# Performance work log

Hardware: AMD Instinct MI355X
Metric: run time of the kernel (lower is better)

The kernel has to match this reference:

```python
import jax, jax.numpy as jnp
import numpy as np

P = 16          # patch size
NUM_HEADS = 8
WINDOW = 64     # window_size from SparseAttention(window_size=64)


def _layer_norm(x, w, b, eps=1e-5):
    mu = jnp.mean(x, axis=-1, keepdims=True)
    var = jnp.var(x, axis=-1, keepdims=True)
    return (x - mu) * jax.lax.rsqrt(var + eps) * w + b


def _sinusoidal_pe(num_patches, num_features, dtype):
    pos = jnp.arange(num_patches, dtype=jnp.float32)[:, None]            # [N,1]
    i = jnp.arange(0, num_features, 2, dtype=jnp.float32)                # [D/2]
    div = jnp.exp(-jnp.log(10000.0) * i / num_features)                  # [D/2]
    ang = pos * div                                                      # [N,D/2]
    pe = jnp.stack([jnp.sin(ang), jnp.cos(ang)], axis=-1).reshape(num_patches, num_features)
    return pe.astype(dtype)


def _ffn(x, w1, b1, w2, b2):
    # FeedForward: Linear -> GELU -> Linear (dropout inactive at eval)
    h = jax.nn.gelu(jnp.einsum('bnd,hd->bnh', x, w1) + b1)
    return jnp.einsum('bnh,dh->bnd', h, w2) + b2


def _windowed_attention(x, qkv_w, qkv_b, proj_w, proj_b):
    B, N, D = x.shape
    hd = D // NUM_HEADS
    qkv = jnp.einsum('bnd,ed->bne', x, qkv_w) + qkv_b                    # [B,N,3D]
    qkv = qkv.reshape(B, N, 3, NUM_HEADS, hd)
    q, k, v = qkv[:, :, 0], qkv[:, :, 1], qkv[:, :, 2]                   # [B,N,H,hd]
    nw = N // WINDOW
    # partition sequence into non-overlapping windows of 64 tokens
    q = q.reshape(B, nw, WINDOW, NUM_HEADS, hd).transpose(0, 3, 1, 2, 4)  # [B,H,nw,W,hd]
    k = k.reshape(B, nw, WINDOW, NUM_HEADS, hd).transpose(0, 3, 1, 2, 4)
    v = v.reshape(B, nw, WINDOW, NUM_HEADS, hd).transpose(0, 3, 1, 2, 4)
    scale = 1.0 / jnp.sqrt(jnp.asarray(hd, x.dtype))
    scores = jnp.einsum('bhwqd,bhwkd->bhwqk', q, k) * scale              # [B,H,nw,W,W]
    attn = jax.nn.softmax(scores, axis=-1)
    out = jnp.einsum('bhwqk,bhwkd->bhwqd', attn, v)                      # [B,H,nw,W,hd]
    out = out.transpose(0, 2, 3, 1, 4).reshape(B, N, D)
    return jnp.einsum('bnd,ed->bne', out, proj_w) + proj_b


def setup_inputs() -> dict:
    key = jax.random.key(0)
    ks = jax.random.split(key, 8)
    D, HF = 256, 1024
    s = lambda fan: 1.0 / np.sqrt(fan)
    return {
        'x': jax.random.normal(ks[0], (32, 3, 512, 512), jnp.float32),
        'conv_w': jax.random.normal(ks[1], (D, 3, P, P), jnp.float32) * s(3 * P * P),
        'conv_b': jnp.zeros((D,), jnp.float32),
        'ln_w': jnp.ones((D,), jnp.float32),
        'ln_b': jnp.zeros((D,), jnp.float32),
        'qkv_w': jax.random.normal(ks[2], (3 * D, D), jnp.float32) * s(D),
        'qkv_b': jnp.zeros((3 * D,), jnp.float32),
        'proj_w': jax.random.normal(ks[3], (D, D), jnp.float32) * s(D),
        'proj_b': jnp.zeros((D,), jnp.float32),
        'ff_w1': jax.random.normal(ks[4], (HF, D), jnp.float32) * s(D),
        'ff_b1': jnp.zeros((HF,), jnp.float32),
        'ff_w2': jax.random.normal(ks[5], (D, HF), jnp.float32) * s(HF),
        'ff_b2': jnp.zeros((D,), jnp.float32),
    }


def reference(x, conv_w, conv_b, ln_w, ln_b, qkv_w, qkv_b, proj_w, proj_b,
              ff_w1, ff_b1, ff_w2, ff_b2):
    B, C, H, W = x.shape
    D = conv_w.shape[0]
    # PatchEmbedding1: Conv2d(C, D, kernel=16, stride=16) == per-patch matmul, then LayerNorm
    nH, nW = H // P, W // P
    patches = x.reshape(B, C, nH, P, nW, P).transpose(0, 2, 4, 1, 3, 5).reshape(B, nH * nW, C * P * P)
    h = jnp.einsum('bnp,dp->bnd', patches, conv_w.reshape(D, -1)) + conv_b
    h = _layer_norm(h, ln_w, ln_b)
    # static sinusoidal position embedding
    h = h + _sinusoidal_pe(h.shape[1], D, h.dtype)
    # block 1: FFN -> sparse (windowed) attention -> residual
    identity = h
    h = _ffn(h, ff_w1, ff_b1, ff_w2, ff_b2)
    h = _windowed_attention(h, qkv_w, qkv_b, proj_w, proj_b)
    h = h + identity
    # block 2: shared FFN -> residual
    identity = h
    h = _ffn(h, ff_w1, ff_b1, ff_w2, ff_b2)
    return h + identity
```

## Files before the change

### kernel.cpp

```cpp
#include <hip/hip_runtime.h>
#include <math.h>


#define M_TOK 32768

typedef __attribute__((ext_vector_type(8))) short  short8;
typedef __attribute__((ext_vector_type(4))) float  f32x4;
typedef __attribute__((ext_vector_type(8))) unsigned short us8v;
typedef __attribute__((ext_vector_type(4))) unsigned short us4v;

__device__ __forceinline__ unsigned short f2b(float f) {
    union { float f; unsigned u; } c; c.f = f;
    unsigned r = c.u + 0x7fffu + ((c.u >> 16) & 1u);
    return (unsigned short)(r >> 16);
}
__device__ __forceinline__ float gelu_fast(float x) {
    const float c0 = 0.7978845608028654f;
    const float c1 = 0.044715f * 0.7978845608028654f;
    float z = x * (c0 + c1 * x * x);
    float e = __expf(-2.0f * z);
    return x * __builtin_amdgcn_rcpf(1.0f + e);
}
__device__ __forceinline__ void load_lds16(const unsigned short* g, void* lds) {
    __builtin_amdgcn_global_load_lds(
        (const __attribute__((address_space(1))) unsigned int*)g,
        (__attribute__((address_space(3))) unsigned int*)lds, 16, 0, 0);
}

__global__ __launch_bounds__(256) void cvt_f2b_kernel(
    const float* __restrict__ in, unsigned short* __restrict__ out, int n)
{
    int i = (blockIdx.x * 256 + threadIdx.x) * 4;
    if (i >= n) return;
    float4 v = *(const float4*)(in + i);
    us4v o;
    o[0] = f2b(v.x); o[1] = f2b(v.y); o[2] = f2b(v.z); o[3] = f2b(v.w);
    *(us4v*)(out + i) = o;
}

__global__ __launch_bounds__(256) void pe_init_kernel(float* __restrict__ pe)
{
    const int pos = blockIdx.x;
    const int d   = threadIdx.x;
    const int ieven = d & ~1;
    float div = expf(-9.210340371976184f * (float)ieven * (1.0f / 256.0f));
    float ang = (float)pos * div;
    pe[pos * 256 + d] = (d & 1) ? cosf(ang) : sinf(ang);
}

template<bool GELU, bool RES, bool WF32, bool WB16>
__global__ __launch_bounds__(256) void mfma_gemm_kernel(
    const unsigned short* __restrict__ A, const unsigned short* __restrict__ W,
    const float* __restrict__ bias, const float* __restrict__ res,
    float* __restrict__ outF, unsigned short* __restrict__ outB,
    int M, int N, int K)
{
    __shared__ unsigned short As[128 * 32];
    __shared__ unsigned short Ws[128 * 32];

    const int t    = threadIdx.x;
    const int m0   = blockIdx.x * 128;
    const int n0   = blockIdx.y * 128;
    const int wv   = t >> 6, lane = t & 63;
    const int wr   = (wv >> 1) * 64, wc = (wv & 1) * 64;
    const int l15  = lane & 15, quad = lane >> 4;

    f32x4 acc[4][4];
#pragma unroll
    for (int i = 0; i < 4; i++)
#pragma unroll
        for (int j = 0; j < 4; j++)
#pragma unroll
            for (int r = 0; r < 4; r++) acc[i][j][r] = 0.0f;

    const int srow = wv * 16 + (lane >> 2);
    const int skk  = (lane & 3) * 8;
    const unsigned short* gA0 = A + (size_t)(m0 + srow) * K + skk;
    const unsigned short* gA1 = gA0 + (size_t)64 * K;
    const unsigned short* gW0 = W + (size_t)(n0 + srow) * K + skk;
    const unsigned short* gW1 = gW0 + (size_t)64 * K;
    char* lA0 = (char*)As + wv * 1024;
    char* lA1 = lA0 + 4096;
    char* lW0 = (char*)Ws + wv * 1024;
    char* lW1 = lW0 + 4096;

    for (int k0 = 0; k0 < K; k0 += 32) {
        __syncthreads();
        load_lds16(gA0 + k0, lA0);
        load_lds16(gA1 + k0, lA1);
        load_lds16(gW0 + k0, lW0);
        load_lds16(gW1 + k0, lW1);
        __syncthreads();

        short8 af[4], wf[4];
#pragma unroll
        for (int i = 0; i < 4; i++)
            af[i] = *(const short8*)&As[(wr + i * 16 + l15) * 32 + quad * 8];
#pragma unroll
        for (int j = 0; j < 4; j++)
            wf[j] = *(const short8*)&Ws[(wc + j * 16 + l15) * 32 + quad * 8];
#pragma unroll
        for (int i = 0; i < 4; i++)
#pragma unroll
            for (int j = 0; j < 4; j++)
                acc[i][j] = __builtin_amdgcn_mfma_f32_16x16x32_bf16(
                    af[i], wf[j], acc[i][j], 0, 0, 0);
    }

#pragma unroll
    for (int i = 0; i < 4; i++) {
        const int gr = m0 + wr + i * 16 + quad * 4;
#pragma unroll
        for (int j = 0; j < 4; j++) {
            const int gc = n0 + wc + j * 16 + l15;
            const float bv = bias[gc];
#pragma unroll
            for (int r = 0; r < 4; r++) {
                float v = acc[i][j][r] + bv;
                if (GELU) v = gelu_fast(v);
                if (RES)  v += res[(size_t)(gr + r) * N + gc];
                if (WF32) outF[(size_t)(gr + r) * N + gc] = v;
                if (WB16) outB[(size_t)(gr + r) * N + gc] = f2b(v);
            }
        }
    }
}

__global__ __launch_bounds__(256) void patch_mfma_kernel(
    const unsigned short* __restrict__ xb, const unsigned short* __restrict__ W,
    const float* __restrict__ bias, float* __restrict__ outF)
{
    __shared__ unsigned short As[128 * 32];
    __shared__ unsigned short Ws[128 * 32];

    const int t    = threadIdx.x;
    const int m0   = blockIdx.x * 128;
    const int n0   = blockIdx.y * 128;
    const int wv   = t >> 6, lane = t & 63;
    const int wr   = (wv >> 1) * 64, wc = (wv & 1) * 64;
    const int l15  = lane & 15, quad = lane >> 4;

    f32x4 acc[4][4];
#pragma unroll
    for (int i = 0; i < 4; i++)
#pragma unroll
        for (int j = 0; j < 4; j++)
#pragma unroll
            for (int r = 0; r < 4; r++) acc[i][j][r] = 0.0f;

    const int srow = wv * 16 + (lane >> 2);
    const int skk  = (lane & 3) * 8;
    size_t xoff[2];
#pragma unroll
    for (int s = 0; s < 2; s++) {
        const int m  = m0 + s * 64 + srow;
        const int b  = m >> 10;
        const int idx = m & 1023;
        const int hh = idx >> 5, ww = idx & 31;
        xoff[s] = ((size_t)(b * 3) * 512 + (size_t)(hh * 16)) * 512 + ww * 16;
    }
    const unsigned short* gW0 = W + (size_t)(n0 + srow) * 768 + skk;
    const unsigned short* gW1 = gW0 + (size_t)64 * 768;
    char* lA0 = (char*)As + wv * 1024;
    char* lA1 = lA0 + 4096;
    char* lW0 = (char*)Ws + wv * 1024;
    char* lW1 = lW0 + 4096;

    for (int k0 = 0; k0 < 768; k0 += 32) {
        const int k  = k0 + skk;
        const int c  = k >> 8;
        const int ph = (k >> 4) & 15;
        const int pw = k & 15;
        const size_t koff = (size_t)c * 262144 + (size_t)ph * 512 + pw;
        __syncthreads();
        load_lds16(xb + xoff[0] + koff, lA0);
        load_lds16(xb + xoff[1] + koff, lA1);
        load_lds16(gW0 + k0, lW0);
        load_lds16(gW1 + k0, lW1);
        __syncthreads();

        short8 af[4], wf[4];
#pragma unroll
        for (int i = 0; i < 4; i++)
            af[i] = *(const short8*)&As[(wr + i * 16 + l15) * 32 + quad * 8];
#pragma unroll
        for (int j = 0; j < 4; j++)
            wf[j] = *(const short8*)&Ws[(wc + j * 16 + l15) * 32 + quad * 8];
#pragma unroll
        for (int i = 0; i < 4; i++)
#pragma unroll
            for (int j = 0; j < 4; j++)
                acc[i][j] = __builtin_amdgcn_mfma_f32_16x16x32_bf16(
                    af[i], wf[j], acc[i][j], 0, 0, 0);
    }

#pragma unroll
    for (int i = 0; i < 4; i++) {
        const int gr = m0 + wr + i * 16 + quad * 4;
#pragma unroll
        for (int j = 0; j < 4; j++) {
            const int gc = n0 + wc + j * 16 + l15;
            const float bv = bias[gc];
#pragma unroll
            for (int r = 0; r < 4; r++)
                outF[(size_t)(gr + r) * 256 + gc] = acc[i][j][r] + bv;
        }
    }
}

__global__ __launch_bounds__(256) void ln_pe_kernel(
    const float* __restrict__ in, const float* __restrict__ w,
    const float* __restrict__ b, const float* __restrict__ pe_t,
    float* __restrict__ outF, unsigned short* __restrict__ outB)
{
    const int m = blockIdx.x;
    const int d = threadIdx.x;
    float v = in[(size_t)m * 256 + d];

    float s = v, s2 = v * v;
#pragma unroll
    for (int off = 32; off > 0; off >>= 1) {
        s  += __shfl_down(s,  off, 64);
        s2 += __shfl_down(s2, off, 64);
    }
    __shared__ float ss[4], ss2[4], stats[2];
    const int lane = d & 63, wid = d >> 6;
    if (lane == 0) { ss[wid] = s; ss2[wid] = s2; }
    __syncthreads();
    if (d == 0) {
        float a  = ss[0] + ss[1] + ss[2] + ss[3];
        float a2 = ss2[0] + ss2[1] + ss2[2] + ss2[3];
        float mean = a * (1.0f / 256.0f);
        float var  = a2 * (1.0f / 256.0f) - mean * mean;
        stats[0] = mean;
        stats[1] = rsqrtf(var + 1e-5f);
    }
    __syncthreads();
    const float mean = stats[0], rstd = stats[1];

    const int pos = m & 1023;
    float pe = pe_t[pos * 256 + d];

    float o = (v - mean) * rstd * w[d] + b[d] + pe;
    outF[(size_t)m * 256 + d] = o;
    outB[(size_t)m * 256 + d] = f2b(o);
}

__global__ __launch_bounds__(256) void attn_mfma_kernel(
    const unsigned short* __restrict__ qkv, unsigned short* __restrict__ out)
{
    __shared__ unsigned short Ps[64 * 72];
    __shared__ unsigned short Vt[32 * 72];

    const int blk = blockIdx.x;
    const int h = blk & 7;
    const int w = (blk >> 3) & 15;
    const int b = blk >> 7;
    const int m_base = b * 1024 + w * 64;

    const int t = threadIdx.x;
    const int wv = t >> 6, lane = t & 63;
    const int l15 = lane & 15, quad = lane >> 4;

    {
        const int row = t >> 2;
        const int c0  = (t & 3) * 8;
        const unsigned short* src = qkv + (size_t)(m_base + row) * 768 + 512 + h * 32 + c0;
        us8v v = *(const us8v*)src;
#pragma unroll
        for (int j = 0; j < 8; j++) Vt[(c0 + j) * 72 + row] = v[j];
    }

    short8 aq = *(const short8*)(qkv + (size_t)(m_base + wv * 16 + l15) * 768 + h * 32 + quad * 8);
    f32x4 c[4];
#pragma unroll
    for (int j = 0; j < 4; j++) {
        short8 bk = *(const short8*)(qkv + (size_t)(m_base + j * 16 + l15) * 768 + 256 + h * 32 + quad * 8);
        f32x4 z = {0.0f, 0.0f, 0.0f, 0.0f};
        c[j] = __builtin_amdgcn_mfma_f32_16x16x32_bf16(aq, bk, z, 0, 0, 0);
    }

    const float scale = 0.17677669529663687f;
    float sm[4];
#pragma unroll
    for (int r = 0; r < 4; r++) {
        float m0 = -1e30f;
#pragma unroll
        for (int j = 0; j < 4; j++) { c[j][r] *= scale; m0 = fmaxf(m0, c[j][r]); }
#pragma unroll
        for (int d = 1; d < 16; d <<= 1) m0 = fmaxf(m0, __shfl_xor(m0, d, 64));
        float s0 = 0.0f;
#pragma unroll
        for (int j = 0; j < 4; j++) { float e = __expf(c[j][r] - m0); c[j][r] = e; s0 += e; }
#pragma unroll
        for (int d = 1; d < 16; d <<= 1) s0 += __shfl_xor(s0, d, 64);
        sm[r] = __builtin_amdgcn_rcpf(s0);
    }

#pragma unroll
    for (int r = 0; r < 4; r++) {
        const int prow = wv * 16 + quad * 4 + r;
#pragma unroll
        for (int j = 0; j < 4; j++)
            Ps[prow * 72 + j * 16 + l15] = f2b(c[j][r] * sm[r]);
    }
    __syncthreads();

    short8 ap0 = *(const short8*)&Ps[(wv * 16 + l15) * 72 + quad * 8];
    short8 ap1 = *(const short8*)&Ps[(wv * 16 + l15) * 72 + 32 + quad * 8];
    f32x4 o[2];
#pragma unroll
    for (int nt = 0; nt < 2; nt++) {
        short8 bv0 = *(const short8*)&Vt[(nt * 16 + l15) * 72 + quad * 8];
        short8 bv1 = *(const short8*)&Vt[(nt * 16 + l15) * 72 + 32 + quad * 8];
        f32x4 z = {0.0f, 0.0f, 0.0f, 0.0f};
        o[nt] = __builtin_amdgcn_mfma_f32_16x16x32_bf16(ap0, bv0, z, 0, 0, 0);
        o[nt] = __builtin_amdgcn_mfma_f32_16x16x32_bf16(ap1, bv1, o[nt], 0, 0, 0);
    }

#pragma unroll
    for (int nt = 0; nt < 2; nt++) {
#pragma unroll
        for (int r = 0; r < 4; r++) {
            const int row = m_base + wv * 16 + quad * 4 + r;
            out[(size_t)row * 256 + h * 32 + nt * 16 + l15] = f2b(o[nt][r]);
        }
    }
}

extern "C" void kernel_launch(void* const* d_in, const int* in_sizes, int n_in,
                              void* d_out, int out_size, void* d_ws, size_t ws_size,
                              hipStream_t stream)
{
    const float* x      = (const float*)d_in[0];
    const float* conv_w = (const float*)d_in[1];
    const float* conv_b = (const float*)d_in[2];
    const float* ln_w   = (const float*)d_in[3];
    const float* ln_b   = (const float*)d_in[4];
    const float* qkv_w  = (const float*)d_in[5];
    const float* qkv_b  = (const float*)d_in[6];
    const float* proj_w = (const float*)d_in[7];
    const float* proj_b = (const float*)d_in[8];
    const float* ff_w1  = (const float*)d_in[9];
    const float* ff_b1  = (const float*)d_in[10];
    const float* ff_w2  = (const float*)d_in[11];
    const float* ff_b2  = (const float*)d_in[12];
    float* out = (float*)d_out;

    char* ws = (char*)d_ws;
    unsigned short* xb    = (unsigned short*)(ws);
    unsigned short* hidb  = (unsigned short*)(ws);
    float*          h0    = (float*)(ws + 67108864);
    unsigned short* qkvb  = (unsigned short*)(ws + 67108864);
    float*          pe_t  = (float*)(ws + 100663296);
    float*          h1f   = (float*)(ws + 117440512);
    unsigned short* h1b   = (unsigned short*)(ws + 150994944);
    unsigned short* aob   = (unsigned short*)(ws + 150994944);
    unsigned short* f1b   = (unsigned short*)(ws + 167772160);
    unsigned short* h2b   = (unsigned short*)(ws + 167772160);
    unsigned short* wbase = (unsigned short*)(ws + 184549376);
    unsigned short* conv_wb = wbase;
    unsigned short* qkv_wb  = wbase + 196608;
    unsigned short* proj_wb = wbase + 393216;
    unsigned short* ff_w1b  = wbase + 458752;
    unsigned short* ff_w2b  = wbase + 720896;

    const int M = M_TOK;
    dim3 blk(256);

    cvt_f2b_kernel<<<dim3(25165824 / 1024), blk, 0, stream>>>(x, xb, 25165824);
    cvt_f2b_kernel<<<dim3(196608 / 1024), blk, 0, stream>>>(conv_w, conv_wb, 196608);
    cvt_f2b_kernel<<<dim3(196608 / 1024), blk, 0, stream>>>(qkv_w, qkv_wb, 196608);
    cvt_f2b_kernel<<<dim3(65536 / 1024), blk, 0, stream>>>(proj_w, proj_wb, 65536);
    cvt_f2b_kernel<<<dim3(262144 / 1024), blk, 0, stream>>>(ff_w1, ff_w1b, 262144);
    cvt_f2b_kernel<<<dim3(262144 / 1024), blk, 0, stream>>>(ff_w2, ff_w2b, 262144);
    pe_init_kernel<<<dim3(1024), blk, 0, stream>>>(pe_t);

    patch_mfma_kernel<<<dim3(M / 128, 2), blk, 0, stream>>>(xb, conv_wb, conv_b, h0);
    ln_pe_kernel<<<dim3(M), blk, 0, stream>>>(h0, ln_w, ln_b, pe_t, h1f, h1b);
    mfma_gemm_kernel<true, false, false, true><<<dim3(M / 128, 8), blk, 0, stream>>>(
        h1b, ff_w1b, ff_b1, nullptr, nullptr, hidb, M, 1024, 256);
    mfma_gemm_kernel<false, false, false, true><<<dim3(M / 128, 2), blk, 0, stream>>>(
        hidb, ff_w2b, ff_b2, nullptr, nullptr, f1b, M, 256, 1024);
    mfma_gemm_kernel<false, false, false, true><<<dim3(M / 128, 6), blk, 0, stream>>>(
        f1b, qkv_wb, qkv_b, nullptr, nullptr, qkvb, M, 768, 256);
    attn_mfma_kernel<<<dim3(4096), blk, 0, stream>>>(qkvb, aob);
    mfma_gemm_kernel<false, true, true, true><<<dim3(M / 128, 2), blk, 0, stream>>>(
        aob, proj_wb, proj_b, h1f, out, h2b, M, 256, 256);
    mfma_gemm_kernel<true, false, false, true><<<dim3(M / 128, 8), blk, 0, stream>>>(
        h2b, ff_w1b, ff_b1, nullptr, nullptr, hidb, M, 1024, 256);
    mfma_gemm_kernel<false, true, true, false><<<dim3(M / 128, 2), blk, 0, stream>>>(
        hidb, ff_w2b, ff_b2, out, out, nullptr, M, 256, 1024);
}
```

Baseline: 436.4 us.

## Swap MFMA operands for vectorized epilogue stores and keep intermediates in bf16

Measured after the change: 467.1 us. +7.0%, slower.

```diff
diff --git a/kernel.cpp b/kernel.cpp
--- a/kernel.cpp
+++ b/kernel.cpp
@@ -13,6 +13,10 @@
     union { float f; unsigned u; } c; c.f = f;
     unsigned r = c.u + 0x7fffu + ((c.u >> 16) & 1u);
     return (unsigned short)(r >> 16);
+}
+__device__ __forceinline__ float b2f(unsigned short u) {
+    union { unsigned u; float f; } c; c.u = ((unsigned)u) << 16;
+    return c.f;
 }
 __device__ __forceinline__ float gelu_fast(float x) {
     const float c0 = 0.7978845608028654f;
@@ -51,7 +55,7 @@
 template<bool GELU, bool RES, bool WF32, bool WB16>
 __global__ __launch_bounds__(256) void mfma_gemm_kernel(
     const unsigned short* __restrict__ A, const unsigned short* __restrict__ W,
-    const float* __restrict__ bias, const float* __restrict__ res,
+    const float* __restrict__ bias, const unsigned short* __restrict__ res,
     float* __restrict__ outF, unsigned short* __restrict__ outB,
     int M, int N, int K)
 {
@@ -59,8 +63,8 @@
     __shared__ unsigned short Ws[128 * 32];
 
     const int t    = threadIdx.x;
-    const int m0   = blockIdx.x * 128;
-    const int n0   = blockIdx.y * 128;
+    const int m0   = blockIdx.y * 128;
+    const int n0   = blockIdx.x * 128;
     const int wv   = t >> 6, lane = t & 63;
     const int wr   = (wv >> 1) * 64, wc = (wv & 1) * 64;
     const int l15  = lane & 15, quad = lane >> 4;
@@ -104,23 +108,37 @@
 #pragma unroll
             for (int j = 0; j < 4; j++)
                 acc[i][j] = __builtin_amdgcn_mfma_f32_16x16x32_bf16(
-                    af[i], wf[j], acc[i][j], 0, 0, 0);
+                    wf[j], af[i], acc[i][j], 0, 0, 0);
     }
 
 #pragma unroll
     for (int i = 0; i < 4; i++) {
-        const int gr = m0 + wr + i * 16 + quad * 4;
+        const int gr = m0 + wr + i * 16 + l15;
 #pragma unroll
         for (int j = 0; j < 4; j++) {
-            const int gc = n0 + wc + j * 16 + l15;
-            const float bv = bias[gc];
-#pragma unroll
-            for (int r = 0; r < 4; r++) {
-                float v = acc[i][j][r] + bv;
-                if (GELU) v = gelu_fast(v);
-                if (RES)  v += res[(size_t)(gr + r) * N + gc];
-                if (WF32) outF[(size_t)(gr + r) * N + gc] = v;
-                if (WB16) outB[(size_t)(gr + r) * N + gc] = f2b(v);
+            const int gc = n0 + wc + j * 16 + quad * 4;
+            const float4 bv = *(const float4*)&bias[gc];
+            float v0 = acc[i][j][0] + bv.x;
+            float v1 = acc[i][j][1] + bv.y;
+            float v2 = acc[i][j][2] + bv.z;
+            float v3 = acc[i][j][3] + bv.w;
+            if (GELU) {
+                v0 = gelu_fast(v0); v1 = gelu_fast(v1);
+                v2 = gelu_fast(v2); v3 = gelu_fast(v3);
+            }
+            if (RES) {
+                us4v rv = *(const us4v*)&res[(size_t)gr * N + gc];
+                v0 += b2f(rv[0]); v1 += b2f(rv[1]);
+                v2 += b2f(rv[2]); v3 += b2f(rv[3]);
+            }
+            if (WF32) {
+                float4 o; o.x = v0; o.y = v1; o.z = v2; o.w = v3;
+                *(float4*)&outF[(size_t)gr * N + gc] = o;
+            }
+            if (WB16) {
+                us4v o;
+                o[0] = f2b(v0); o[1] = f2b(v1); o[2] = f2b(v2); o[3] = f2b(v3);
+                *(us4v*)&outB[(size_t)gr * N + gc] = o;
             }
         }
     }
@@ -128,14 +146,14 @@
 
 __global__ __launch_bounds__(256) void patch_mfma_kernel(
     const unsigned short* __restrict__ xb, const unsigned short* __restrict__ W,
-    const float* __restrict__ bias, float* __restrict__ outF)
+    const float* __restrict__ bias, unsigned short* __restrict__ outB)
 {
     __shared__ unsigned short As[128 * 32];
     __shared__ unsigned short Ws[128 * 32];
 
     const int t    = threadIdx.x;
-    const int m0   = blockIdx.x * 128;
-    const int n0   = blockIdx.y * 128;
+    const int m0   = blockIdx.y * 128;
+    const int n0   = blockIdx.x * 128;
     const int wv   = t >> 6, lane = t & 63;
     const int wr   = (wv >> 1) * 64, wc = (wv & 1) * 64;
     const int l15  = lane & 15, quad = lane >> 4;
@@ -191,31 +209,34 @@
 #pragma unroll
             for (int j = 0; j < 4; j++)
                 acc[i][j] = __builtin_amdgcn_mfma_f32_16x16x32_bf16(
-                    af[i], wf[j], acc[i][j], 0, 0, 0);
+                    wf[j], af[i], acc[i][j], 0, 0, 0);
     }
 
 #pragma unroll
     for (int i = 0; i < 4; i++) {
-        const int gr = m0 + wr + i * 16 + quad * 4;
+        const int gr = m0 + wr + i * 16 + l15;
 #pragma unroll
         for (int j = 0; j < 4; j++) {
-            const int gc = n0 + wc + j * 16 + l15;
-            const float bv = bias[gc];
-#pragma unroll
-            for (int r = 0; r < 4; r++)
-                outF[(size_t)(gr + r) * 256 + gc] = acc[i][j][r] + bv;
+            const int gc = n0 + wc + j * 16 + quad * 4;
+            const float4 bv = *(const float4*)&bias[gc];
+            us4v o;
+            o[0] = f2b(acc[i][j][0] + bv.x);
+            o[1] = f2b(acc[i][j][1] + bv.y);
+            o[2] = f2b(acc[i][j][2] + bv.z);
+            o[3] = f2b(acc[i][j][3] + bv.w);
+            *(us4v*)&outB[(size_t)gr * 256 + gc] = o;
         }
     }
 }
 
 __global__ __launch_bounds__(256) void ln_pe_kernel(
-    const float* __restrict__ in, const float* __restrict__ w,
+    const unsigned short* __restrict__ in, const float* __restrict__ w,
     const float* __restrict__ b, const float* __restrict__ pe_t,
-    float* __restrict__ outF, unsigned short* __restrict__ outB)
+    unsigned short* __restrict__ outB)
 {
     const int m = blockIdx.x;
     const int d = threadIdx.x;
-    float v = in[(size_t)m * 256 + d];
+    float v = b2f(in[(size_t)m * 256 + d]);
 
     float s = v, s2 = v * v;
 #pragma unroll
@@ -242,7 +263,6 @@
     float pe = pe_t[pos * 256 + d];
 
     float o = (v - mean) * rstd * w[d] + b[d] + pe;
-    outF[(size_t)m * 256 + d] = o;
     outB[(size_t)m * 256 + d] = f2b(o);
 }
 
@@ -350,15 +370,14 @@
     char* ws = (char*)d_ws;
     unsigned short* xb    = (unsigned short*)(ws);
     unsigned short* hidb  = (unsigned short*)(ws);
-    float*          h0    = (float*)(ws + 67108864);
+    unsigned short* h0b   = (unsigned short*)(ws + 67108864);
     unsigned short* qkvb  = (unsigned short*)(ws + 67108864);
-    float*          pe_t  = (float*)(ws + 100663296);
-    float*          h1f   = (float*)(ws + 117440512);
-    unsigned short* h1b   = (unsigned short*)(ws + 150994944);
-    unsigned short* aob   = (unsigned short*)(ws + 150994944);
-    unsigned short* f1b   = (unsigned short*)(ws + 167772160);
-    unsigned short* h2b   = (unsigned short*)(ws + 167772160);
-    unsigned short* wbase = (unsigned short*)(ws + 184549376);
+    float*          pe_t  = (float*)(ws + 117440512);
+    unsigned short* h1b   = (unsigned short*)(ws + 118489088);
+    unsigned short* f1b   = (unsigned short*)(ws + 135266304);
+    unsigned short* h2b   = (unsigned short*)(ws + 152043520);
+    unsigned short* aob   = (unsigned short*)(ws + 168820736);
+    unsigned short* wbase = (unsigned short*)(ws + 185597952);
     unsigned short* conv_wb = wbase;
     unsigned short* qkv_wb  = wbase + 196608;
     unsigned short* proj_wb = wbase + 393216;
@@ -376,19 +395,19 @@
     cvt_f2b_kernel<<<dim3(262144 / 1024), blk, 0, stream>>>(ff_w2, ff_w2b, 262144);
     pe_init_kernel<<<dim3(1024), blk, 0, stream>>>(pe_t);
 
-    patch_mfma_kernel<<<dim3(M / 128, 2), blk, 0, stream>>>(xb, conv_wb, conv_b, h0);
-    ln_pe_kernel<<<dim3(M), blk, 0, stream>>>(h0, ln_w, ln_b, pe_t, h1f, h1b);
-    mfma_gemm_kernel<true, false, false, true><<<dim3(M / 128, 8), blk, 0, stream>>>(
+    patch_mfma_kernel<<<dim3(2, M / 128), blk, 0, stream>>>(xb, conv_wb, conv_b, h0b);
+    ln_pe_kernel<<<dim3(M), blk, 0, stream>>>(h0b, ln_w, ln_b, pe_t, h1b);
+    mfma_gemm_kernel<true, false, false, true><<<dim3(8, M / 128), blk, 0, stream>>>(
         h1b, ff_w1b, ff_b1, nullptr, nullptr, hidb, M, 1024, 256);
-    mfma_gemm_kernel<false, false, false, true><<<dim3(M / 128, 2), blk, 0, stream>>>(
+    mfma_gemm_kernel<false, false, false, true><<<dim3(2, M / 128), blk, 0, stream>>>(
         hidb, ff_w2b, ff_b2, nullptr, nullptr, f1b, M, 256, 1024);
-    mfma_gemm_kernel<false, false, false, true><<<dim3(M / 128, 6), blk, 0, stream>>>(
+    mfma_gemm_kernel<false, false, false, true><<<dim3(6, M / 128), blk, 0, stream>>>(
         f1b, qkv_wb, qkv_b, nullptr, nullptr, qkvb, M, 768, 256);
     attn_mfma_kernel<<<dim3(4096), blk, 0, stream>>>(qkvb, aob);
-    mfma_gemm_kernel<false, true, true, true><<<dim3(M / 128, 2), blk, 0, stream>>>(
-        aob, proj_wb, proj_b, h1f, out, h2b, M, 256, 256);
-    mfma_gemm_kernel<true, false, false, true><<<dim3(M / 128, 8), blk, 0, stream>>>(
+    mfma_gemm_kernel<false, true, false, true><<<dim3(2, M / 128), blk, 0, stream>>>(
+        aob, proj_wb, proj_b, h1b, nullptr, h2b, M, 256, 256);
+    mfma_gemm_kernel<true, false, false, true><<<dim3(8, M / 128), blk, 0, stream>>>(
         h2b, ff_w1b, ff_b1, nullptr, nullptr, hidb, M, 1024, 256);
-    mfma_gemm_kernel<false, true, true, false><<<dim3(M / 128, 2), blk, 0, stream>>>(
-        hidb, ff_w2b, ff_b2, out, out, nullptr, M, 256, 1024);
-}
+    mfma_gemm_kernel<false, true, true, false><<<dim3(2, M / 128), blk, 0, stream>>>(
+        hidb, ff_w2b, ff_b2, h2b, out, nullptr, M, 256, 1024);
+}
```
